# Kernel tuning notes

Hardware: AMD Instinct MI355X
Metric: run time of the kernel (lower is better)

## Reference

```python
import jax, jax.numpy as jnp
import numpy as np

VOCAB, VDIM, DDIM, BATCH = 50257, 300, 512, 16


def setup_inputs() -> dict:
    key = jax.random.key(0)
    k1, k2, k3, k4, k5 = jax.random.split(key, 5)
    return {
        "decoder_hidden": jax.random.normal(k1, (BATCH, DDIM), dtype=jnp.float32),
        "embedding_vocab": jax.random.normal(k2, (VOCAB, VDIM), dtype=jnp.float32),
        "W_dec": jax.random.normal(k3, (VDIM, DDIM), dtype=jnp.float32) * (1.0 / np.sqrt(DDIM)),
        "b_dec": jax.random.normal(k4, (VDIM,), dtype=jnp.float32) * 0.01,
        "W_full": jax.random.normal(k5, (VDIM,), dtype=jnp.float32) * (1.0 / np.sqrt(VDIM)),
        "b_full": jnp.zeros((), dtype=jnp.float32),
    }


def reference(decoder_hidden, embedding_vocab, W_dec, b_dec, W_full, b_full):
    # query: (B, vocab_dim) = decoder_att(decoder_hidden)
    query = decoder_hidden @ W_dec.T + b_dec
    # additive scores: relu(vocab + query) projected to scalar -> (B, V)
    hidden = jax.nn.relu(embedding_vocab[None, :, :] + query[:, None, :])  # (B, V, D)
    att = jnp.einsum("bvd,d->bv", hidden, W_full) + b_full
    alpha = jax.nn.softmax(att, axis=1)  # softmax over vocab
    # weighted sum of vocab embeddings: (B, vocab_dim)
    attention_weighted_encoding = jnp.einsum("bv,vd->bd", alpha, embedding_vocab)
    return attention_weighted_encoding, alpha
```

## Files before the change

kernel.cpp:

```cpp
#include <hip/hip_runtime.h>

constexpr int V  = 50257;
constexpr int D  = 300;
constexpr int KD = 512;
constexpr int B  = 16;

constexpr int ROWS = 64;
constexpr int NB_ATT = (V + ROWS - 1) / ROWS;
constexpr int NT = 5;
constexpr int NC  = 512;
constexpr int RPC = (V + NC - 1) / NC;

constexpr float NEG_HUGE = -1.0e30f;

constexpr size_t WS_QT   = 0;
constexpr size_t WS_STAT = 4800;
constexpr size_t WS_MS   = WS_STAT + (size_t)NB_ATT * 32;
constexpr size_t WS_PART = WS_MS + 32;
constexpr size_t WS_TMP  = WS_PART + (size_t)NC * 4800;

struct f4 { float v[4]; };
__device__ __forceinline__ f4 ld4(const float* p) {
    float4 t = *(const float4*)p;
    return {t.x, t.y, t.z, t.w};
}

#define AS1 __attribute__((address_space(1)))
#define AS3 __attribute__((address_space(3)))
#define DPPF(x, CTRL) __int_as_float(__builtin_amdgcn_mov_dpp(__float_as_int(x), (CTRL), 0xF, 0xF, false))

__global__ void __launch_bounds__(256) k_query(
    const float* __restrict__ dh, const float* __restrict__ Wdec,
    const float* __restrict__ bdec, float* __restrict__ q_t)
{
    int wid  = (blockIdx.x * 256 + threadIdx.x) >> 6;
    int lane = threadIdx.x & 63;
    if (wid >= D * B) return;
    int d = wid >> 4, b = wid & 15;
    const float* wrow = Wdec + (size_t)d * KD;
    const float* hrow = dh + (size_t)b * KD;
    float s = 0.f;
    for (int k = lane; k < KD; k += 64) s += wrow[k] * hrow[k];
    #pragma unroll
    for (int off = 32; off; off >>= 1) s += __shfl_down(s, off, 64);
    if (lane == 0) q_t[d * 16 + b] = s + bdec[d];
}

__global__ void __launch_bounds__(256, 3) k_att(
    const float* __restrict__ E, const float* __restrict__ q_t,
    const float* __restrict__ wf, const float* __restrict__ bf,
    float* __restrict__ att, float* __restrict__ blkstats)
{
    __shared__ float se[2 * 4096];
    __shared__ float sq[5120];

    const int t    = threadIdx.x;
    const int slot = t & 15;
    const int rg   = t >> 4;
    const int s4   = slot << 2;
    const int v0   = blockIdx.x * ROWS;

    for (int i = t; i < 5120; i += 256) {
        int d = i >> 4, b = i & 15;
        int bq = b >> 2, bl = b & 3;
        float v = (d < D) ? q_t[d * 16 + b] : 0.f;
        int P = (d >> 1) * 8 + ((((d & 1) << 2) | bq) ^ ((d >> 2) & 7));
        sq[P * 4 + bl] = v;
    }

    f4 wreg[NT];
    #pragma unroll
    for (int k = 0; k < NT; ++k)
        #pragma unroll
        for (int i = 0; i < 4; ++i) {
            int d = k * 64 + s4 + i;
            wreg[k].v[i] = (d < D) ? wf[d] : 0.f;
        }

    int xq[2][4];
    #pragma unroll
    for (int i1 = 0; i1 < 2; ++i1)
        #pragma unroll
        for (int bq = 0; bq < 4; ++bq)
            xq[i1][bq] = slot * 64 + 4 * ((((i1 << 2) | bq)) ^ (slot & 7));

    float acc[4][16];
    #pragma unroll
    for (int j = 0; j < 4; ++j)
        #pragma unroll
        for (int b = 0; b < 16; ++b) acc[j][b] = 0.f;

#define STAGE(TT, BI) do {                                                    \
    int dd = (TT) * 64 + s4;                                                  \
    if (dd >= D) dd = 0;                         \
    _Pragma("unroll")                                                         \
    for (int jj = 0; jj < 4; ++jj) {                                          \
        int row = v0 + jj * 16 + rg;                                          \
        if (row >= V) row = V - 1;                                            \
        const float* src = E + (size_t)row * D + dd;                          \
        float* lb = se + (BI) * 4096 + jj * 1024 + (t << 2);                  \
        __builtin_amdgcn_global_load_lds((const AS1 void*)src,                \
                                         (AS3 void*)lb, 16, 0, 0);            \
    }                                                                         \
} while (0)

#define COMPUTE(TT, BI) do {                                                  \
    const float* buf = se + (BI) * 4096;                                      \
    f4 ej[4];                                                                 \
    _Pragma("unroll")                                                         \
    for (int j = 0; j < 4; ++j) ej[j] = ld4(buf + j * 1024 + (t << 2));       \
    const float* sqt = sq + (TT) * 1024;                                      \
    _Pragma("unroll")                                                         \
    for (int i = 0; i < 4; ++i) {                                             \
        float wi = wreg[TT].v[i];                                             \
        _Pragma("unroll")                                                     \
        for (int bq = 0; bq < 4; ++bq) {                                      \
            f4 qv = ld4(sqt + (i >> 1) * 32 + xq[i & 1][bq]);                 \
            _Pragma("unroll")                                                 \
            for (int j = 0; j < 4; ++j) {                                     \
                float e = ej[j].v[i];                                         \
                _Pragma("unroll")                                             \
                for (int bl = 0; bl < 4; ++bl)                                \
                    acc[j][bq * 4 + bl] =                                     \
                        fmaf(fmaxf(e + qv.v[bl], 0.f), wi,                    \
                             acc[j][bq * 4 + bl]);                            \
            }                                                                 \
        }                                                                     \
    }                                                                         \
} while (0)

    STAGE(0, 0);
    asm volatile("s_waitcnt vmcnt(0)" ::: "memory");
    __syncthreads();

    #pragma unroll
    for (int tt = 0; tt < NT; ++tt) {
        if (tt + 1 < NT) STAGE(tt + 1, (tt + 1) & 1);
        COMPUTE(tt, tt & 1);
        asm volatile("s_waitcnt vmcnt(0)" ::: "memory");
        __builtin_amdgcn_s_barrier();
        __builtin_amdgcn_sched_barrier(0);
    }
#undef STAGE
#undef COMPUTE

    #pragma unroll
    for (int j = 0; j < 4; ++j)
        #pragma unroll
        for (int b = 0; b < 16; ++b) {
            float x = acc[j][b];
            x += DPPF(x, 0xB1);
            x += DPPF(x, 0x4E);
            acc[j][b] = x;
        }
    const int c = slot & 3;
    float kept[4][4];
    #pragma unroll
    for (int j = 0; j < 4; ++j)
        #pragma unroll
        for (int kk = 0; kk < 4; ++kk) {
            float x = (c == 0) ? acc[j][kk]
                    : (c == 1) ? acc[j][4 + kk]
                    : (c == 2) ? acc[j][8 + kk]
                    :            acc[j][12 + kk];
            x += __shfl_xor(x, 4, 64);
            x += __shfl_xor(x, 8, 64);
            kept[j][kk] = x;
        }

    __syncthreads();
    float* smsM = se;
    float* smsS = se + 1024;

    const float bfull = bf[0];
    const int g = (t >> 6) * 16 + (rg & 3) * 4 + (slot >> 2);
    const int jown = slot >> 2;
    const int rowown = v0 + rg + 16 * jown;
    const bool okown = rowown < V;

    #pragma unroll
    for (int kk = 0; kk < 4; ++kk) {
        const int b = 4 * c + kk;
        float x = ((jown == 0) ? kept[0][kk] : (jown == 1) ? kept[1][kk]
                 : (jown == 2) ? kept[2][kk] : kept[3][kk]) + bfull;
        if (okown) att[(size_t)b * V + rowown] = x;
        smsM[g * 16 + b] = okown ? x : NEG_HUGE;
        smsS[g * 16 + b] = okown ? 1.f : 0.f;
    }
    __syncthreads();
    if (t < 64) {
        int b = t & 15, q4 = t >> 4;
        float m = NEG_HUGE, s = 0.f;
        for (int u = 0; u < 16; ++u) {
            int gg = q4 * 16 + u;
            float mg = smsM[gg * 16 + b], sg = smsS[gg * 16 + b];
            float mn = fmaxf(m, mg);
            s = s * __expf(m - mn) + sg * __expf(mg - mn);
            m = mn;
        }
        se[2048 + q4 * 16 + b] = m;
        se[2112 + q4 * 16 + b] = s;
    }
    __syncthreads();
    if (t < 16) {
        float m = NEG_HUGE, s = 0.f;
        #pragma unroll
        for (int q4 = 0; q4 < 4; ++q4) {
            float mg = se[2048 + q4 * 16 + t], sg = se[2112 + q4 * 16 + t];
            float mn = fmaxf(m, mg);
            s = s * __expf(m - mn) + sg * __expf(mg - mn);
            m = mn;
        }
        blkstats[((size_t)blockIdx.x * 16 + t) * 2]     = m;
        blkstats[((size_t)blockIdx.x * 16 + t) * 2 + 1] = s;
    }
}

__global__ void __launch_bounds__(64) k_combine(
    const float* __restrict__ blkstats, float* __restrict__ MS)
{
    int b = blockIdx.x, lane = threadIdx.x;
    float m = NEG_HUGE;
    for (int cc = lane; cc < NB_ATT; cc += 64)
        m = fmaxf(m, blkstats[(size_t)(cc * 16 + b) * 2]);
    #pragma unroll
    for (int off = 32; off; off >>= 1) m = fmaxf(m, __shfl_xor(m, off, 64));
    float s = 0.f;
    for (int cc = lane; cc < NB_ATT; cc += 64)
        s += blkstats[(size_t)(cc * 16 + b) * 2 + 1] *
             __expf(blkstats[(size_t)(cc * 16 + b) * 2] - m);
    #pragma unroll
    for (int off = 32; off; off >>= 1) s += __shfl_xor(s, off, 64);
    if (lane == 0) { MS[b * 2] = m; MS[b * 2 + 1] = 1.f / s; }
}

__global__ void __launch_bounds__(320) k_awsum(
    const float* __restrict__ E, float* __restrict__ att,
    const float* __restrict__ MS, float* __restrict__ partials)
{
    __shared__ float sal[RPC * 16];
    int c = blockIdx.x, t = threadIdx.x;
    int v0 = c * RPC;
    int n = V - v0;
    if (n > RPC) n = RPC;
    if (n < 0) n = 0;

    for (int i = t; i < RPC * 16; i += 320) {
        int b = i / RPC, vv = i - b * RPC;
        float a = 0.f;
        if (vv < n) {
            float M = MS[b * 2], invS = MS[b * 2 + 1];
            size_t gi = (size_t)b * V + v0 + vv;
            a = __expf(att[gi] - M) * invS;
            att[gi] = a;
        }
        sal[vv * 16 + b] = a;
    }
    __syncthreads();

    if (t < D) {
        float acc[16];
        #pragma unroll
        for (int b = 0; b < 16; ++b) acc[b] = 0.f;
        #pragma unroll 4
        for (int vv = 0; vv < n; ++vv) {
            float e = E[(size_t)(v0 + vv) * D + t];
            const float* ap = sal + vv * 16;
            f4 a0 = ld4(ap), a1 = ld4(ap + 4), a2 = ld4(ap + 8), a3 = ld4(ap + 12);
            #pragma unroll
            for (int b = 0; b < 4; ++b) {
                acc[b]      = fmaf(a0.v[b], e, acc[b]);
                acc[b + 4]  = fmaf(a1.v[b], e, acc[b + 4]);
                acc[b + 8]  = fmaf(a2.v[b], e, acc[b + 8]);
                acc[b + 12] = fmaf(a3.v[b], e, acc[b + 12]);
            }
        }
        #pragma unroll
        for (int b = 0; b < 16; ++b)
            partials[(size_t)c * 4800 + b * D + t] = acc[b];
    }
}

__global__ void __launch_bounds__(256) k_red1(
    const float* __restrict__ partials, float* __restrict__ tmp)
{
    int o4 = blockIdx.x * 256 + threadIdx.x;
    if (o4 >= 1200) return;
    int y = blockIdx.y;
    float4 s = {0.f, 0.f, 0.f, 0.f};
    for (int c = y * 32; c < y * 32 + 32; ++c) {
        float4 p = *(const float4*)(partials + (size_t)c * 4800 + o4 * 4);
        s.x += p.x; s.y += p.y; s.z += p.z; s.w += p.w;
    }
    *(float4*)(tmp + (size_t)y * 4800 + o4 * 4) = s;
}

__global__ void __launch_bounds__(256) k_red2(
    const float* __restrict__ tmp, float* __restrict__ out)
{
    int o4 = blockIdx.x * 256 + threadIdx.x;
    if (o4 >= 1200) return;
    float4 s = {0.f, 0.f, 0.f, 0.f};
    #pragma unroll
    for (int y = 0; y < 16; ++y) {
        float4 p = *(const float4*)(tmp + (size_t)y * 4800 + o4 * 4);
        s.x += p.x; s.y += p.y; s.z += p.z; s.w += p.w;
    }
    *(float4*)(out + o4 * 4) = s;
}

extern "C" void kernel_launch(void* const* d_in, const int* in_sizes, int n_in,
                              void* d_out, int out_size, void* d_ws, size_t ws_size,
                              hipStream_t stream) {
    const float* dh   = (const float*)d_in[0];
    const float* E    = (const float*)d_in[1];
    const float* Wdec = (const float*)d_in[2];
    const float* bdec = (const float*)d_in[3];
    const float* wf   = (const float*)d_in[4];
    const float* bf   = (const float*)d_in[5];
    float* out = (float*)d_out;
    float* ws  = (float*)d_ws;

    float* q_t   = ws + WS_QT;
    float* stats = ws + WS_STAT;
    float* MS    = ws + WS_MS;
    float* part  = ws + WS_PART;
    float* tmp   = ws + WS_TMP;
    float* att   = out + 4800;

    k_query<<<(D * B + 3) / 4, 256, 0, stream>>>(dh, Wdec, bdec, q_t);
    k_att<<<NB_ATT, 256, 0, stream>>>(E, q_t, wf, bf, att, stats);
    k_combine<<<B, 64, 0, stream>>>(stats, MS);
    k_awsum<<<NC, 320, 0, stream>>>(E, att, MS, part);
    k_red1<<<dim3(5, 16), 256, 0, stream>>>(part, tmp);
    k_red2<<<5, 256, 0, stream>>>(tmp, out);
}
```

Before: 87.11 us.

## Halve attention tile rows, bulk-load tile to LDS, pre-swizzle query, pack FP32 math

The attention kernel now handles 32 vocab rows per block. It loads the whole contiguous embedding tile into LDS in one shot instead of using a double-buffered per-chunk pipeline. The query kernel writes q already in the LDS swizzled layout, so k_att copies it directly with global_load_lds. The inner ReLU-FMA loop uses 2-wide vector types to target packed FP32 instructions, and the in-block softmax stat reduction is simplified. The weighted-sum kernel is retuned to 448 chunks with deeper unroll. The trade-off is twice as many blocks, which doubles the per-block q staging and stats traffic, and no overlap between loads and compute.

```diff
diff --git a/kernel.cpp b/kernel.cpp
--- a/kernel.cpp
+++ b/kernel.cpp
@@ -5,19 +5,21 @@
 constexpr int KD = 512;
 constexpr int B  = 16;
 
-constexpr int ROWS = 64;
+constexpr int ROWS = 32;
 constexpr int NB_ATT = (V + ROWS - 1) / ROWS;
 constexpr int NT = 5;
-constexpr int NC  = 512;
-constexpr int RPC = (V + NC - 1) / NC;
+constexpr int NC  = 448;
+constexpr int RPC = 113;
 
 constexpr float NEG_HUGE = -1.0e30f;
 
 constexpr size_t WS_QT   = 0;
-constexpr size_t WS_STAT = 4800;
+constexpr size_t WS_STAT = 5120;
 constexpr size_t WS_MS   = WS_STAT + (size_t)NB_ATT * 32;
 constexpr size_t WS_PART = WS_MS + 32;
 constexpr size_t WS_TMP  = WS_PART + (size_t)NC * 4800;
+
+typedef float v2f __attribute__((ext_vector_type(2)));
 
 struct f4 { float v[4]; };
 __device__ __forceinline__ f4 ld4(const float* p) {
@@ -31,121 +33,124 @@
 
 __global__ void __launch_bounds__(256) k_query(
     const float* __restrict__ dh, const float* __restrict__ Wdec,
-    const float* __restrict__ bdec, float* __restrict__ q_t)
+    const float* __restrict__ bdec, float* __restrict__ q_swz)
 {
     int wid  = (blockIdx.x * 256 + threadIdx.x) >> 6;
     int lane = threadIdx.x & 63;
-    if (wid >= D * B) return;
+    if (wid >= 320 * 16) return;
     int d = wid >> 4, b = wid & 15;
-    const float* wrow = Wdec + (size_t)d * KD;
-    const float* hrow = dh + (size_t)b * KD;
     float s = 0.f;
-    for (int k = lane; k < KD; k += 64) s += wrow[k] * hrow[k];
-    #pragma unroll
-    for (int off = 32; off; off >>= 1) s += __shfl_down(s, off, 64);
-    if (lane == 0) q_t[d * 16 + b] = s + bdec[d];
-}
-
-__global__ void __launch_bounds__(256, 3) k_att(
-    const float* __restrict__ E, const float* __restrict__ q_t,
+    if (d < D) {
+        const float* wrow = Wdec + (size_t)d * KD;
+        const float* hrow = dh + (size_t)b * KD;
+        for (int k = lane; k < KD; k += 64) s += wrow[k] * hrow[k];
+        #pragma unroll
+        for (int off = 32; off; off >>= 1) s += __shfl_down(s, off, 64);
+        s += bdec[d];
+    }
+    if (lane == 0) {
+        int P = (d >> 1) * 8 + ((((d & 1) << 2) | (b >> 2)) ^ ((d >> 2) & 7));
+        q_swz[P * 4 + (b & 3)] = (d < D) ? s : 0.f;
+    }
+}
+
+__global__ void __launch_bounds__(256) k_att(
+    const float* __restrict__ E, const float* __restrict__ q_swz,
     const float* __restrict__ wf, const float* __restrict__ bf,
     float* __restrict__ att, float* __restrict__ blkstats)
 {
-    __shared__ float se[2 * 4096];
-    __shared__ float sq[5120];
+    __shared__ __align__(16) float sq[5120];
+    __shared__ __align__(16) float seE[9632];
+    __shared__ float sms[768];
 
     const int t    = threadIdx.x;
     const int slot = t & 15;
     const int rg   = t >> 4;
-    const int s4   = slot << 2;
     const int v0   = blockIdx.x * ROWS;
 
-    for (int i = t; i < 5120; i += 256) {
-        int d = i >> 4, b = i & 15;
-        int bq = b >> 2, bl = b & 3;
-        float v = (d < D) ? q_t[d * 16 + b] : 0.f;
-        int P = (d >> 1) * 8 + ((((d & 1) << 2) | bq) ^ ((d >> 2) & 7));
-        sq[P * 4 + bl] = v;
-    }
+    #pragma unroll
+    for (int k = 0; k < 5; ++k)
+        __builtin_amdgcn_global_load_lds((const AS1 void*)(q_swz + k * 1024 + t * 4),
+                                         (AS3 void*)(sq + k * 1024 + t * 4), 16, 0, 0);
+    int nrow = V - v0; if (nrow > ROWS) nrow = ROWS;
+    const int nflt = nrow * 300;
+    const float* Eb = E + (size_t)v0 * 300;
+    #pragma unroll
+    for (int k = 0; k < 10; ++k) {
+        int o = k * 1024 + t * 4;
+        if (o < nflt)
+            __builtin_amdgcn_global_load_lds((const AS1 void*)(Eb + o),
+                                             (AS3 void*)(seE + o), 16, 0, 0);
+    }
+    if (t < 32) seE[9600 + t] = 0.f;
 
     f4 wreg[NT];
     #pragma unroll
-    for (int k = 0; k < NT; ++k)
+    for (int k = 0; k < 4; ++k) wreg[k] = ld4(wf + k * 64 + slot * 4);
+    if (slot < 11) wreg[4] = ld4(wf + 256 + slot * 4);
+    else { wreg[4].v[0] = wreg[4].v[1] = wreg[4].v[2] = wreg[4].v[3] = 0.f; }
+    #pragma unroll
+    for (int i = 0; i < 4; ++i)
+        if (256 + slot * 4 + i >= D && slot < 11) wreg[4].v[i] = 0.f;
+    const float bfull = bf[0];
+
+    int xq[2][4];
+    #pragma unroll
+    for (int i1 = 0; i1 < 2; ++i1)
+        #pragma unroll
+        for (int bq = 0; bq < 4; ++bq)
+            xq[i1][bq] = slot * 64 + 4 * (((i1 << 2) | bq) ^ (slot & 7));
+
+    v2f acc2[2][8];
+    #pragma unroll
+    for (int j = 0; j < 2; ++j)
+        #pragma unroll
+        for (int p = 0; p < 8; ++p) acc2[j][p] = (v2f){0.f, 0.f};
+
+    __syncthreads();
+
+    #pragma unroll
+    for (int tt = 0; tt < NT; ++tt) {
+        f4 e0 = ld4(seE + rg * 300 + tt * 64 + slot * 4);
+        f4 e1 = ld4(seE + (rg + 16) * 300 + tt * 64 + slot * 4);
+        const float* sqt = sq + tt * 1024;
         #pragma unroll
         for (int i = 0; i < 4; ++i) {
-            int d = k * 64 + s4 + i;
-            wreg[k].v[i] = (d < D) ? wf[d] : 0.f;
-        }
-
-    int xq[2][4];
-    #pragma unroll
-    for (int i1 = 0; i1 < 2; ++i1)
-        #pragma unroll
-        for (int bq = 0; bq < 4; ++bq)
-            xq[i1][bq] = slot * 64 + 4 * ((((i1 << 2) | bq)) ^ (slot & 7));
-
-    float acc[4][16];
-    #pragma unroll
-    for (int j = 0; j < 4; ++j)
-        #pragma unroll
-        for (int b = 0; b < 16; ++b) acc[j][b] = 0.f;
-
-#define STAGE(TT, BI) do {                                                    \
-    int dd = (TT) * 64 + s4;                                                  \
-    if (dd >= D) dd = 0;                         \
-    _Pragma("unroll")                                                         \
-    for (int jj = 0; jj < 4; ++jj) {                                          \
-        int row = v0 + jj * 16 + rg;                                          \
-        if (row >= V) row = V - 1;                                            \
-        const float* src = E + (size_t)row * D + dd;                          \
-        float* lb = se + (BI) * 4096 + jj * 1024 + (t << 2);                  \
-        __builtin_amdgcn_global_load_lds((const AS1 void*)src,                \
-                                         (AS3 void*)lb, 16, 0, 0);            \
-    }                                                                         \
-} while (0)
-
-#define COMPUTE(TT, BI) do {                                                  \
-    const float* buf = se + (BI) * 4096;                                      \
-    f4 ej[4];                                                                 \
-    _Pragma("unroll")                                                         \
-    for (int j = 0; j < 4; ++j) ej[j] = ld4(buf + j * 1024 + (t << 2));       \
-    const float* sqt = sq + (TT) * 1024;                                      \
-    _Pragma("unroll")                                                         \
-    for (int i = 0; i < 4; ++i) {                                             \
-        float wi = wreg[TT].v[i];                                             \
-        _Pragma("unroll")                                                     \
-        for (int bq = 0; bq < 4; ++bq) {                                      \
-            f4 qv = ld4(sqt + (i >> 1) * 32 + xq[i & 1][bq]);                 \
-            _Pragma("unroll")                                                 \
-            for (int j = 0; j < 4; ++j) {                                     \
-                float e = ej[j].v[i];                                         \
-                _Pragma("unroll")                                             \
-                for (int bl = 0; bl < 4; ++bl)                                \
-                    acc[j][bq * 4 + bl] =                                     \
-                        fmaf(fmaxf(e + qv.v[bl], 0.f), wi,                    \
-                             acc[j][bq * 4 + bl]);                            \
-            }                                                                 \
-        }                                                                     \
-    }                                                                         \
-} while (0)
-
-    STAGE(0, 0);
-    asm volatile("s_waitcnt vmcnt(0)" ::: "memory");
-    __syncthreads();
-
-    #pragma unroll
-    for (int tt = 0; tt < NT; ++tt) {
-        if (tt + 1 < NT) STAGE(tt + 1, (tt + 1) & 1);
-        COMPUTE(tt, tt & 1);
-        asm volatile("s_waitcnt vmcnt(0)" ::: "memory");
-        __builtin_amdgcn_s_barrier();
-        __builtin_amdgcn_sched_barrier(0);
-    }
-#undef STAGE
-#undef COMPUTE
-
-    #pragma unroll
-    for (int j = 0; j < 4; ++j)
+            float wi = wreg[tt].v[i];
+            v2f w2 = {wi, wi};
+            #pragma unroll
+            for (int bq = 0; bq < 4; ++bq) {
+                f4 qv = ld4(sqt + (i >> 1) * 32 + xq[i & 1][bq]);
+                v2f qlo = {qv.v[0], qv.v[1]};
+                v2f qhi = {qv.v[2], qv.v[3]};
+                v2f z2  = {0.f, 0.f};
+                v2f ea  = {e0.v[i], e0.v[i]};
+                v2f lo0 = __builtin_elementwise_max(ea + qlo, z2);
+                v2f hi0 = __builtin_elementwise_max(ea + qhi, z2);
+                acc2[0][bq*2]   = __builtin_elementwise_fma(lo0, w2, acc2[0][bq*2]);
+                acc2[0][bq*2+1] = __builtin_elementwise_fma(hi0, w2, acc2[0][bq*2+1]);
+                v2f eb  = {e1.v[i], e1.v[i]};
+                v2f lo1 = __builtin_elementwise_max(eb + qlo, z2);
+                v2f hi1 = __builtin_elementwise_max(eb + qhi, z2);
+                acc2[1][bq*2]   = __builtin_elementwise_fma(lo1, w2, acc2[1][bq*2]);
+                acc2[1][bq*2+1] = __builtin_elementwise_fma(hi1, w2, acc2[1][bq*2+1]);
+            }
+        }
+    }
+
+    float acc[2][16];
+    #pragma unroll
+    for (int j = 0; j < 2; ++j)
+        #pragma unroll
+        for (int bq = 0; bq < 4; ++bq) {
+            acc[j][bq*4+0] = acc2[j][bq*2][0];
+            acc[j][bq*4+1] = acc2[j][bq*2][1];
+            acc[j][bq*4+2] = acc2[j][bq*2+1][0];
+            acc[j][bq*4+3] = acc2[j][bq*2+1][1];
+        }
+
+    #pragma unroll
+    for (int j = 0; j < 2; ++j)
         #pragma unroll
         for (int b = 0; b < 16; ++b) {
             float x = acc[j][b];
@@ -154,9 +159,9 @@
             acc[j][b] = x;
         }
     const int c = slot & 3;
-    float kept[4][4];
-    #pragma unroll
-    for (int j = 0; j < 4; ++j)
+    float kept[2][4];
+    #pragma unroll
+    for (int j = 0; j < 2; ++j)
         #pragma unroll
         for (int kk = 0; kk < 4; ++kk) {
             float x = (c == 0) ? acc[j][kk]
@@ -168,45 +173,38 @@
             kept[j][kk] = x;
         }
 
+    const int jown = (slot >> 2) & 1;
+    const int dup  = slot >> 3;
+    const int row  = v0 + rg + 16 * jown;
+    const bool ok  = row < V;
+    const int g    = rg + 16 * jown;
+    #pragma unroll
+    for (int kk2 = 0; kk2 < 2; ++kk2) {
+        int b = 4 * c + (dup ? 2 : 0) + kk2;
+        float x0 = jown ? kept[1][kk2]     : kept[0][kk2];
+        float x1 = jown ? kept[1][2 + kk2] : kept[0][2 + kk2];
+        float x  = (dup ? x1 : x0) + bfull;
+        if (ok) att[(size_t)b * V + row] = x;
+        sms[g * 16 + b] = ok ? x : NEG_HUGE;
+    }
     __syncthreads();
-    float* smsM = se;
-    float* smsS = se + 1024;
-
-    const float bfull = bf[0];
-    const int g = (t >> 6) * 16 + (rg & 3) * 4 + (slot >> 2);
-    const int jown = slot >> 2;
-    const int rowown = v0 + rg + 16 * jown;
-    const bool okown = rowown < V;
-
-    #pragma unroll
-    for (int kk = 0; kk < 4; ++kk) {
-        const int b = 4 * c + kk;
-        float x = ((jown == 0) ? kept[0][kk] : (jown == 1) ? kept[1][kk]
-                 : (jown == 2) ? kept[2][kk] : kept[3][kk]) + bfull;
-        if (okown) att[(size_t)b * V + rowown] = x;
-        smsM[g * 16 + b] = okown ? x : NEG_HUGE;
-        smsS[g * 16 + b] = okown ? 1.f : 0.f;
-    }
-    __syncthreads();
-    if (t < 64) {
-        int b = t & 15, q4 = t >> 4;
-        float m = NEG_HUGE, s = 0.f;
-        for (int u = 0; u < 16; ++u) {
-            int gg = q4 * 16 + u;
-            float mg = smsM[gg * 16 + b], sg = smsS[gg * 16 + b];
-            float mn = fmaxf(m, mg);
-            s = s * __expf(m - mn) + sg * __expf(mg - mn);
-            m = mn;
-        }
-        se[2048 + q4 * 16 + b] = m;
-        se[2112 + q4 * 16 + b] = s;
+    if (t < 128) {
+        int b = t & 15, gq = t >> 4;
+        float m = NEG_HUGE;
+        #pragma unroll
+        for (int u = 0; u < 4; ++u) m = fmaxf(m, sms[(gq * 4 + u) * 16 + b]);
+        float s = 0.f;
+        #pragma unroll
+        for (int u = 0; u < 4; ++u) s += __expf(sms[(gq * 4 + u) * 16 + b] - m);
+        sms[512 + gq * 16 + b] = m;
+        sms[640 + gq * 16 + b] = s;
     }
     __syncthreads();
     if (t < 16) {
         float m = NEG_HUGE, s = 0.f;
         #pragma unroll
-        for (int q4 = 0; q4 < 4; ++q4) {
-            float mg = se[2048 + q4 * 16 + t], sg = se[2112 + q4 * 16 + t];
+        for (int gq = 0; gq < 8; ++gq) {
+            float mg = sms[512 + gq * 16 + t], sg = sms[640 + gq * 16 + t];
             float mn = fmaxf(m, mg);
             s = s * __expf(m - mn) + sg * __expf(mg - mn);
             m = mn;
@@ -262,7 +260,7 @@
         float acc[16];
         #pragma unroll
         for (int b = 0; b < 16; ++b) acc[b] = 0.f;
-        #pragma unroll 4
+        #pragma unroll 8
         for (int vv = 0; vv < n; ++vv) {
             float e = E[(size_t)(v0 + vv) * D + t];
             const float* ap = sal + vv * 16;
@@ -288,7 +286,7 @@
     if (o4 >= 1200) return;
     int y = blockIdx.y;
     float4 s = {0.f, 0.f, 0.f, 0.f};
-    for (int c = y * 32; c < y * 32 + 32; ++c) {
+    for (int c = y * 28; c < y * 28 + 28; ++c) {
         float4 p = *(const float4*)(partials + (size_t)c * 4800 + o4 * 4);
         s.x += p.x; s.y += p.y; s.z += p.z; s.w += p.w;
     }
@@ -321,15 +319,15 @@
     float* out = (float*)d_out;
     float* ws  = (float*)d_ws;
 
-    float* q_t   = ws + WS_QT;
+    float* q_swz = ws + WS_QT;
     float* stats = ws + WS_STAT;
     float* MS    = ws + WS_MS;
     float* part  = ws + WS_PART;
     float* tmp   = ws + WS_TMP;
     float* att   = out + 4800;
 
-    k_query<<<(D * B + 3) / 4, 256, 0, stream>>>(dh, Wdec, bdec, q_t);
-    k_att<<<NB_ATT, 256, 0, stream>>>(E, q_t, wf, bf, att, stats);
+    k_query<<<(320 * 16) / 4, 256, 0, stream>>>(dh, Wdec, bdec, q_swz);
+    k_att<<<NB_ATT, 256, 0, stream>>>(E, q_swz, wf, bf, att, stats);
     k_combine<<<B, 64, 0, stream>>>(stats, MS);
     k_awsum<<<NC, 320, 0, stream>>>(E, att, MS, part);
     k_red1<<<dim3(5, 16), 256, 0, stream>>>(part, tmp);
```

After: 74.37 us. 14.6% less time.
